# Optimization experiments

Measured on AMD Instinct MI355X. Metric: run time of the kernel, lower is better.

## Reference

```python
import jax, jax.numpy as jnp
import numpy as np

HIDDEN = 2048
NUM_HEADS = 16
HEAD_DIM = 128
CHUNK = 256
TOPK = 4
THETA = 10000.0
SCALE = HEAD_DIM ** -0.5


def _rope(x, pos):
    # x: [S, H, D], pos: [S] int. NeoX-style rotate-half (vLLM get_rope default).
    half = HEAD_DIM // 2
    inv = 1.0 / (THETA ** (jnp.arange(half, dtype=jnp.float32) / half))
    ang = pos.astype(jnp.float32)[:, None] * inv          # [S, half]
    cos = jnp.cos(ang)[:, None, :]                        # [S, 1, half]
    sin = jnp.sin(ang)[:, None, :]
    x1, x2 = x[..., :half], x[..., half:]
    return jnp.concatenate([x1 * cos - x2 * sin, x2 * cos + x1 * sin], axis=-1)


def _moba_attn(q, k, v):
    # q, k, v: [S, H, D]; causal MoBA block-sparse attention for one sequence.
    S, H, D = q.shape
    N = S // CHUNK
    # mean-pooled key gate per chunk: [N, H, D]
    key_gate = k.reshape(N, CHUNK, H, D).mean(axis=1)
    gate = jnp.einsum('shd,nhd->shn', q, key_gate)        # [S, H, N]
    cq = jnp.arange(S) // CHUNK                           # chunk index of each query
    n_idx = jnp.arange(N)
    neg = jnp.finfo(gate.dtype).min
    future = (n_idx[None, :] > cq[:, None])[:, None, :]   # [S, 1, N]
    selfc = (n_idx[None, :] == cq[:, None])[:, None, :]
    gate = jnp.where(future, neg, gate)
    gate = jnp.where(selfc, jnp.inf, gate)                # self chunk always selected
    k_sel = min(TOPK, N)
    _, idx = jax.lax.top_k(gate, k_sel)                   # [S, H, k]
    sel = jax.nn.one_hot(idx, N, dtype=jnp.float32).sum(axis=-2) > 0  # [S, H, N] bool
    # expand chunk selection to per-key mask and combine with causal mask
    chunk_of_t = jnp.arange(S) // CHUNK
    sel_full = sel[:, :, chunk_of_t]                      # [S, H, S]
    causal = (jnp.arange(S)[None, :] <= jnp.arange(S)[:, None])[:, None, :]
    allow = causal & sel_full
    scores = jnp.einsum('shd,thd->sht', q, k) * SCALE     # [S, H, S]
    scores = jnp.where(allow, scores, neg)
    p = jax.nn.softmax(scores, axis=-1)
    return jnp.einsum('sht,thd->shd', p, v)


def setup_inputs() -> dict:
    key = jax.random.key(0)
    k1, k2, k3 = jax.random.split(key, 3)
    B, S = 2, 2048
    hidden_states = jax.random.normal(k1, (B, S, HIDDEN), dtype=jnp.float32)
    positions = jnp.tile(jnp.arange(S, dtype=jnp.int32)[None, :], (B, 1))
    qkv_w = jax.random.normal(k2, (3 * NUM_HEADS * HEAD_DIM, HIDDEN), dtype=jnp.float32) * 0.02
    o_w = jax.random.normal(k3, (HIDDEN, NUM_HEADS * HEAD_DIM), dtype=jnp.float32) * 0.02
    return {'hidden_states': hidden_states, 'positions': positions, 'qkv_w': qkv_w, 'o_w': o_w}


def reference(hidden_states, positions, qkv_w, o_w):
    B, S, _ = hidden_states.shape
    qkv = jnp.einsum('bsi,oi->bso', hidden_states, qkv_w)  # [B, S, 3*H*D]
    q, k, v = jnp.split(qkv, 3, axis=-1)
    q = q.reshape(B, S, NUM_HEADS, HEAD_DIM)
    k = k.reshape(B, S, NUM_HEADS, HEAD_DIM)
    v = v.reshape(B, S, NUM_HEADS, HEAD_DIM)
    q = jax.vmap(_rope)(q, positions)
    k = jax.vmap(_rope)(k, positions)
    o = jax.vmap(_moba_attn)(q, k, v)                      # [B, S, H, D]
    o = o.reshape(B, S, NUM_HEADS * HEAD_DIM)
    return jnp.einsum('bsd,od->bso', o, o_w)
```

## Files before the change

### kernel.cpp

```cpp
#include <hip/hip_runtime.h>
#include <hip/hip_bf16.h>
#include <math.h>
#include <string.h>

#define SEQ     2048
#define NHEAD   16
#define HDIM    128
#define HIDDEN  2048
#define QKV_N   6144
#define CHUNKSZ 256
#define NCHUNK  8
#define SCALE_F 0.08838834764831845f
#define NEGBIG  -1e30f

typedef unsigned short u16;
typedef unsigned int   u32;
typedef _Float16       f16;
typedef __attribute__((ext_vector_type(8))) short    s16x8;
typedef __attribute__((ext_vector_type(8))) _Float16 f16x8;
typedef __attribute__((ext_vector_type(4))) float    f32x4;

__device__ __forceinline__ u16 f2bf(float x) {
  __hip_bfloat16 h = __float2bfloat16(x);
  u16 r; memcpy(&r, &h, 2); return r;
}
__device__ __forceinline__ float bf2f(u16 u) {
  u32 b = (u32)u << 16; float f; memcpy(&f, &b, 4); return f;
}

__global__ __launch_bounds__(256) void prep_fl(const float* __restrict__ src,
                                               f16* __restrict__ hi,
                                               f16* __restrict__ lo) {
  int idx = blockIdx.x * 256 + threadIdx.x;
  int l  = idx & 63;
  int ks = (idx >> 6) & 63;
  int mt = idx >> 12;
  const float* sp = src + (size_t)(mt * 16 + (l & 15)) * 2048 + ks * 32 + (l >> 4) * 8;
  float4 a = *(const float4*)sp;
  float4 b = *(const float4*)(sp + 4);
  float xs[8] = {a.x, a.y, a.z, a.w, b.x, b.y, b.z, b.w};
  f16x8 hv, lv;
#pragma unroll
  for (int j = 0; j < 8; ++j) {
    _Float16 h = (_Float16)xs[j];
    hv[j] = h;
    lv[j] = (_Float16)((xs[j] - (float)h) * 2048.0f);
  }
  size_t d = (size_t)idx * 8;
  *(f16x8*)&hi[d] = hv;
  *(f16x8*)&lo[d] = lv;
}

__global__ __launch_bounds__(256, 2) void gemm_fl(
    const f16* __restrict__ Ah, const f16* __restrict__ Al,
    const f16* __restrict__ Bh, const f16* __restrict__ Bl,
    float* __restrict__ C, int ldC, int coff) {
  __shared__ __align__(16) f16 sA[2][8][512];
  __shared__ __align__(16) f16 sB[2][8][512];
  const int tid = threadIdx.x;
  const int w = tid >> 6, lane = tid & 63;
  const int wr = w >> 1, wc = w & 1;
  const int lr = lane & 15, lg = lane >> 4;
  const int bm8 = blockIdx.y * 8;
  const int bn8 = blockIdx.x * 8;

  const f16* gmat = (w == 0) ? Ah : (w == 1) ? Al : (w == 2) ? Bh : Bl;
  const int  base8 = (w < 2) ? bm8 : bn8;
  f16* lmat = (w == 0) ? &sA[0][0][0] : (w == 1) ? &sA[1][0][0]
            : (w == 2) ? &sB[0][0][0] : &sB[1][0][0];
  const f16* gw = gmat + (size_t)lane * 8;
  f16* lw = lmat + lane * 8;

  f32x4 accH[4][4], accX[4][4];
#pragma unroll
  for (int i = 0; i < 4; ++i)
#pragma unroll
    for (int j = 0; j < 4; ++j) {
      accH[i][j] = (f32x4){0.f, 0.f, 0.f, 0.f};
      accX[i][j] = (f32x4){0.f, 0.f, 0.f, 0.f};
    }

  for (int ks = 0; ks < 64; ++ks) {
    f16x8 stg[8];
#pragma unroll
    for (int i = 0; i < 8; ++i)
      stg[i] = *(const f16x8*)(gw + (((size_t)(base8 + i) * 64 + ks) << 9));
    __syncthreads();
#pragma unroll
    for (int i = 0; i < 8; ++i)
      *(f16x8*)(lw + (i << 9)) = stg[i];
    __syncthreads();

    f16x8 ah[4], al[4], bh[4], bl[4];
#pragma unroll
    for (int i = 0; i < 4; ++i) {
      ah[i] = *(const f16x8*)&sA[0][wr * 4 + i][lane * 8];
      al[i] = *(const f16x8*)&sA[1][wr * 4 + i][lane * 8];
      bh[i] = *(const f16x8*)&sB[0][wc * 4 + i][lane * 8];
      bl[i] = *(const f16x8*)&sB[1][wc * 4 + i][lane * 8];
    }
#pragma unroll
    for (int i = 0; i < 4; ++i)
#pragma unroll
      for (int j = 0; j < 4; ++j) {
        accH[i][j] = __builtin_amdgcn_mfma_f32_16x16x32_f16(ah[i], bh[j], accH[i][j], 0, 0, 0);
        accX[i][j] = __builtin_amdgcn_mfma_f32_16x16x32_f16(al[i], bh[j], accX[i][j], 0, 0, 0);
        accX[i][j] = __builtin_amdgcn_mfma_f32_16x16x32_f16(ah[i], bl[j], accX[i][j], 0, 0, 0);
      }
  }

#pragma unroll
  for (int i = 0; i < 4; ++i) {
    const int row0 = blockIdx.y * 128 + wr * 64 + i * 16 + lg * 4;
    const int col0 = coff + blockIdx.x * 128 + wc * 64 + lr;
#pragma unroll
    for (int r = 0; r < 4; ++r) {
      float* cp = C + (size_t)(row0 + r) * ldC + col0;
#pragma unroll
      for (int j = 0; j < 4; ++j)
        cp[j * 16] = accH[i][j][r] + accX[i][j][r] * 4.8828125e-4f;
    }
  }
}

__global__ __launch_bounds__(256) void rope_inplace(float* __restrict__ qkv,
                                                    const int* __restrict__ pos) {
  int idx = blockIdx.x * 256 + threadIdx.x;
  int j = idx & 63;
  int h = (idx >> 6) & 15;
  int s = (idx >> 10) & (SEQ - 1);
  int b = idx >> 21;
  float p = (float)pos[b * SEQ + s];
  float inv = (float)exp(-(double)j * 1.4391156831212787e-1);
  float ang = p * inv;
  float sn = sinf(ang);
  float cs = cosf(ang);
  size_t row = (size_t)(b * SEQ + s) * QKV_N;
  float* qp = qkv + row + h * HDIM;
  float x1 = qp[j], x2 = qp[j + 64];
  qp[j] = x1 * cs - x2 * sn;
  qp[j + 64] = x2 * cs + x1 * sn;
  float* kp = qkv + row + HIDDEN + h * HDIM;
  x1 = kp[j]; x2 = kp[j + 64];
  kp[j] = x1 * cs - x2 * sn;
  kp[j + 64] = x2 * cs + x1 * sn;
}

__global__ __launch_bounds__(128) void key_gate_k(const float* __restrict__ qkv,
                                                  float* __restrict__ kg) {
  int bhn = blockIdx.x;
  int d = threadIdx.x;
  int n = bhn & 7;
  int bh = bhn >> 3;
  int b = bh >> 4, h = bh & 15;
  const float* kp = qkv + (size_t)(b * SEQ + n * CHUNKSZ) * QKV_N + HIDDEN + h * HDIM + d;
  float sum = 0.f;
  for (int i = 0; i < CHUNKSZ; ++i) sum += kp[(size_t)i * QKV_N];
  kg[(size_t)bh * NCHUNK * HDIM + n * HDIM + d] = sum * (1.f / CHUNKSZ);
}

__global__ __launch_bounds__(256) void gate_topk(const float* __restrict__ qkv,
                                                 const float* __restrict__ kg,
                                                 unsigned char* __restrict__ msk) {
  int gw = (blockIdx.x * 256 + threadIdx.x) >> 6;
  int lane = threadIdx.x & 63;
  int s = gw & (SEQ - 1);
  int bh = gw >> 11;
  int b = bh >> 4, h = bh & 15;
  int cq = s >> 8;
  const float* qp = qkv + (size_t)(b * SEQ + s) * QKV_N + h * HDIM;
  float q0 = qp[lane], q1 = qp[lane + 64];
  const float* kgp = kg + (size_t)bh * NCHUNK * HDIM;
  float g[7];
#pragma unroll
  for (int n = 0; n < 7; ++n) {
    float part = 0.f;
    if (n < cq) part = q0 * kgp[n * HDIM + lane] + q1 * kgp[n * HDIM + lane + 64];
#pragma unroll
    for (int off = 32; off > 0; off >>= 1) part += __shfl_xor(part, off);
    g[n] = part;
  }
  unsigned m = 1u << cq;
  int nsel = cq < 3 ? cq : 3;
#pragma unroll
  for (int it = 0; it < 3; ++it) {
    int best = -1; float bv = 0.f;
#pragma unroll
    for (int n = 0; n < 7; ++n) {
      bool cand = (n < cq) && !((m >> n) & 1u);
      if (cand && (best < 0 || g[n] > bv)) { bv = g[n]; best = n; }
    }
    if (it < nsel) m |= 1u << best;
  }
  if (lane == 0) msk[gw] = (unsigned char)m;
}

__global__ __launch_bounds__(256) void prep_k(const float* __restrict__ qkv,
                                              u16* __restrict__ khi,
                                              u16* __restrict__ klo) {
  int idx = blockIdx.x * 256 + threadIdx.x;
  int lane = idx & 63;
  int ds = (idx >> 6) & 3;
  int kt = (idx >> 8) & 127;
  int bh = idx >> 15;
  int b = bh >> 4, h = bh & 15;
  int s = kt * 16 + (lane & 15);
  int d = ds * 32 + (lane >> 4) * 8;
  const float* src = qkv + (size_t)(b * SEQ + s) * QKV_N + HIDDEN + h * HDIM + d;
  float4 a = *(const float4*)src;
  float4 c = *(const float4*)(src + 4);
  float xs[8] = {a.x, a.y, a.z, a.w, c.x, c.y, c.z, c.w};
  s16x8 hi, lo;
#pragma unroll
  for (int j = 0; j < 8; ++j) {
    u16 hb = f2bf(xs[j]);
    hi[j] = (short)hb;
    lo[j] = (short)f2bf(xs[j] - bf2f(hb));
  }
  size_t dst = (size_t)idx * 8;
  *(s16x8*)&khi[dst] = hi;
  *(s16x8*)&klo[dst] = lo;
}

__global__ __launch_bounds__(256) void prep_v(const float* __restrict__ qkv,
                                              u16* __restrict__ vhi,
                                              u16* __restrict__ vlo) {
  int idx = blockIdx.x * 256 + threadIdx.x;
  int lane = idx & 63;
  int ts = (idx >> 6) & 63;
  int dt = (idx >> 12) & 7;
  int bh = idx >> 15;
  int b = bh >> 4, h = bh & 15;
  int t = ts * 32 + (lane >> 4) * 8;
  int d = dt * 16 + (lane & 15);
  const float* src = qkv + (size_t)(b * SEQ + t) * QKV_N + 2 * HIDDEN + h * HDIM + d;
  s16x8 hi, lo;
#pragma unroll
  for (int j = 0; j < 8; ++j) {
    float x = src[(size_t)j * QKV_N];
    u16 hb = f2bf(x);
    hi[j] = (short)hb;
    lo[j] = (short)f2bf(x - bf2f(hb));
  }
  size_t dst = (size_t)idx * 8;
  *(s16x8*)&vhi[dst] = hi;
  *(s16x8*)&vlo[dst] = lo;
}

#define PSTRIDE 40
__global__ __launch_bounds__(256) void moba_attn_mfma(
    const float* __restrict__ qkv,
    const u16* __restrict__ khi, const u16* __restrict__ klo,
    const u16* __restrict__ vhi, const u16* __restrict__ vlo,
    const unsigned char* __restrict__ msk, float* __restrict__ o) {
  __shared__ u16 KHI[4096], KLO[4096];
  __shared__ u16 VHI[4096], VLO[4096];
  __shared__ u16 PHI[4][16 * PSTRIDE], PLO[4][16 * PSTRIDE];
  __shared__ unsigned char Ms[64];
  __shared__ unsigned bm_sh;

  const int qt = blockIdx.x, h = blockIdx.y, b = blockIdx.z;
  const int tid = threadIdx.x;
  const int w = tid >> 6, lane = tid & 63;
  const int lr = lane & 15, lg = lane >> 4;
  const int bh = b * NHEAD + h;
  const int q0g = qt * 64;
  const int q0w = q0g + w * 16;
  const int cq = qt >> 2;

  if (tid < 64) Ms[tid] = msk[(size_t)bh * SEQ + q0g + tid];
  __syncthreads();
  if (tid == 0) {
    unsigned m = 0;
    for (int i = 0; i < 64; ++i) m |= Ms[i];
    bm_sh = m;
  }

  s16x8 qh[4], ql[4];
  {
    const float* qp = qkv + (size_t)(b * SEQ + q0w + lr) * QKV_N + h * HDIM + lg * 8;
#pragma unroll
    for (int ds = 0; ds < 4; ++ds) {
      float4 a = *(const float4*)(qp + ds * 32);
      float4 c = *(const float4*)(qp + ds * 32 + 4);
      float xs[8] = {a.x, a.y, a.z, a.w, c.x, c.y, c.z, c.w};
      s16x8 hi, lo;
#pragma unroll
      for (int j = 0; j < 8; ++j) {
        u16 hb = f2bf(xs[j]);
        hi[j] = (short)hb;
        lo[j] = (short)f2bf(xs[j] - bf2f(hb));
      }
      qh[ds] = hi; ql[ds] = lo;
    }
  }
  __syncthreads();
  const unsigned bmask = bm_sh;

  int qrow[4]; unsigned char rowm[4];
#pragma unroll
  for (int r = 0; r < 4; ++r) {
    qrow[r] = q0w + lg * 4 + r;
    rowm[r] = Ms[w * 16 + lg * 4 + r];
  }

  float m_run[4], l_run[4];
  f32x4 Oacc[8];
#pragma unroll
  for (int r = 0; r < 4; ++r) { m_run[r] = NEGBIG; l_run[r] = 0.f; }
#pragma unroll
  for (int dt = 0; dt < 8; ++dt) Oacc[dt] = (f32x4){0.f, 0.f, 0.f, 0.f};

  for (int n = 0; n <= cq; ++n) {
    if (!((bmask >> n) & 1u)) continue;
    const int nk = (n == cq) ? ((qt & 3) * 64 + 64) : CHUNKSZ;
    for (int t0 = n * CHUNKSZ; t0 < n * CHUNKSZ + nk; t0 += 32) {
      __syncthreads();
      if (w < 2) {
        const u16* src = (w == 0 ? khi : klo) +
                         ((size_t)bh * 128 + (t0 >> 4)) * 2048 + lane * 8;
        u16* dst = (w == 0 ? KHI : KLO);
#pragma unroll
        for (int i = 0; i < 8; ++i)
          *(s16x8*)&dst[i * 512 + lane * 8] = *(const s16x8*)(src + i * 512);
      } else {
        const u16* src = (w == 2 ? vhi : vlo) +
                         ((size_t)bh * 8 * 64 + (t0 >> 5)) * 512 + lane * 8;
        u16* dst = (w == 2 ? VHI : VLO);
#pragma unroll
        for (int dt = 0; dt < 8; ++dt)
          *(s16x8*)&dst[dt * 512 + lane * 8] = *(const s16x8*)(src + (size_t)dt * 32768);
      }
      __syncthreads();

      f32x4 acc[2];
      acc[0] = (f32x4){0.f, 0.f, 0.f, 0.f};
      acc[1] = (f32x4){0.f, 0.f, 0.f, 0.f};
#pragma unroll
      for (int kt = 0; kt < 2; ++kt)
#pragma unroll
        for (int ds = 0; ds < 4; ++ds) {
          s16x8 bhf = *(const s16x8*)&KHI[(kt * 4 + ds) * 512 + lane * 8];
          s16x8 blf = *(const s16x8*)&KLO[(kt * 4 + ds) * 512 + lane * 8];
          acc[kt] = __builtin_amdgcn_mfma_f32_16x16x32_bf16(qh[ds], bhf, acc[kt], 0, 0, 0);
          acc[kt] = __builtin_amdgcn_mfma_f32_16x16x32_bf16(ql[ds], bhf, acc[kt], 0, 0, 0);
          acc[kt] = __builtin_amdgcn_mfma_f32_16x16x32_bf16(qh[ds], blf, acc[kt], 0, 0, 0);
        }

      const int tg0 = t0 + lr, tg1 = t0 + 16 + lr;
      float alpha[4], p0v[4], p1v[4];
#pragma unroll
      for (int r = 0; r < 4; ++r) {
        bool okm = (rowm[r] >> n) & 1;
        float a0 = (okm && tg0 <= qrow[r]) ? acc[0][r] * SCALE_F : NEGBIG;
        float a1 = (okm && tg1 <= qrow[r]) ? acc[1][r] * SCALE_F : NEGBIG;
        float mx = fmaxf(a0, a1);
        mx = fmaxf(mx, __shfl_xor(mx, 1));
        mx = fmaxf(mx, __shfl_xor(mx, 2));
        mx = fmaxf(mx, __shfl_xor(mx, 4));
        mx = fmaxf(mx, __shfl_xor(mx, 8));
        float mnew = fmaxf(m_run[r], mx);
        float al = __expf(m_run[r] - mnew);
        float p0 = __expf(a0 - mnew);
        float p1 = __expf(a1 - mnew);
        float ps = p0 + p1;
        ps += __shfl_xor(ps, 1);
        ps += __shfl_xor(ps, 2);
        ps += __shfl_xor(ps, 4);
        ps += __shfl_xor(ps, 8);
        l_run[r] = l_run[r] * al + ps;
        m_run[r] = mnew;
        alpha[r] = al; p0v[r] = p0; p1v[r] = p1;
      }
      f32x4 av = {alpha[0], alpha[1], alpha[2], alpha[3]};
#pragma unroll
      for (int dt = 0; dt < 8; ++dt) Oacc[dt] *= av;

#pragma unroll
      for (int r = 0; r < 4; ++r) {
        int row = lg * 4 + r;
        u16 h0 = f2bf(p0v[r]);
        u16 h1 = f2bf(p1v[r]);
        PHI[w][row * PSTRIDE + lr]      = h0;
        PHI[w][row * PSTRIDE + 16 + lr] = h1;
        PLO[w][row * PSTRIDE + lr]      = f2bf(p0v[r] - bf2f(h0));
        PLO[w][row * PSTRIDE + 16 + lr] = f2bf(p1v[r] - bf2f(h1));
      }
      s16x8 pah = *(const s16x8*)&PHI[w][lr * PSTRIDE + lg * 8];
      s16x8 pal = *(const s16x8*)&PLO[w][lr * PSTRIDE + lg * 8];
#pragma unroll
      for (int dt = 0; dt < 8; ++dt) {
        s16x8 vbh = *(const s16x8*)&VHI[dt * 512 + lane * 8];
        s16x8 vbl = *(const s16x8*)&VLO[dt * 512 + lane * 8];
        Oacc[dt] = __builtin_amdgcn_mfma_f32_16x16x32_bf16(pah, vbh, Oacc[dt], 0, 0, 0);
        Oacc[dt] = __builtin_amdgcn_mfma_f32_16x16x32_bf16(pal, vbh, Oacc[dt], 0, 0, 0);
        Oacc[dt] = __builtin_amdgcn_mfma_f32_16x16x32_bf16(pah, vbl, Oacc[dt], 0, 0, 0);
      }
    }
  }

  float inv[4];
#pragma unroll
  for (int r = 0; r < 4; ++r) inv[r] = 1.f / l_run[r];
#pragma unroll
  for (int dt = 0; dt < 8; ++dt)
#pragma unroll
    for (int r = 0; r < 4; ++r)
      o[(size_t)(b * SEQ + qrow[r]) * HIDDEN + h * HDIM + dt * 16 + lr] =
          Oacc[dt][r] * inv[r];
}

extern "C" void kernel_launch(void* const* d_in, const int* in_sizes, int n_in,
                              void* d_out, int out_size, void* d_ws, size_t ws_size,
                              hipStream_t stream) {
  const float* hs    = (const float*)d_in[0];
  const int*   pos   = (const int*)d_in[1];
  const float* w_qkv = (const float*)d_in[2];
  const float* w_o   = (const float*)d_in[3];
  float* out = (float*)d_out;

  char* ws = (char*)d_ws;
  float* qkv = (float*)ws;
  float* o   = (float*)(ws + 100663296);
  float* kg  = (float*)(ws + 134217728);
  unsigned char* msk = (unsigned char*)(ws + 134348800);
  char* rx   = ws + 134414336;
  f16* Ah = (f16*)rx;
  f16* Al = (f16*)(rx + 16777216);
  f16* Bh = (f16*)(rx + 33554432);
  f16* Bl = (f16*)(rx + 41943040);
  u16* khi = (u16*)rx;
  u16* klo = (u16*)(rx + 16777216);
  u16* vhi = (u16*)(rx + 33554432);
  u16* vlo = (u16*)(rx + 50331648);

  prep_fl<<<4096, 256, 0, stream>>>(hs, Ah, Al);
  for (int i = 0; i < 3; ++i) {
    prep_fl<<<2048, 256, 0, stream>>>(w_qkv + (size_t)i * 2048 * 2048, Bh, Bl);
    gemm_fl<<<dim3(16, 32), 256, 0, stream>>>(Ah, Al, Bh, Bl, qkv, QKV_N, i * 2048);
  }
  rope_inplace<<<16384, 256, 0, stream>>>(qkv, pos);
  key_gate_k<<<2 * NHEAD * NCHUNK, 128, 0, stream>>>(qkv, kg);
  gate_topk<<<16384, 256, 0, stream>>>(qkv, kg, msk);
  prep_k<<<4096, 256, 0, stream>>>(qkv, khi, klo);
  prep_v<<<4096, 256, 0, stream>>>(qkv, vhi, vlo);
  moba_attn_mfma<<<dim3(SEQ / 64, NHEAD, 2), 256, 0, stream>>>(qkv, khi, klo,
                                                               vhi, vlo, msk, o);
  prep_fl<<<4096, 256, 0, stream>>>(o, Ah, Al);
  prep_fl<<<2048, 256, 0, stream>>>(w_o, Bh, Bl);
  gemm_fl<<<dim3(16, 32), 256, 0, stream>>>(Ah, Al, Bh, Bl, out, HIDDEN, 0);
}
```

Measured before the change: 972.6 us.

## Prefetch next K/V tile into registers, remap attention grid for XCD locality

```diff
diff --git a/kernel.cpp b/kernel.cpp
--- a/kernel.cpp
+++ b/kernel.cpp
@@ -259,7 +259,13 @@
   __shared__ unsigned char Ms[64];
   __shared__ unsigned bm_sh;
 
-  const int qt = blockIdx.x, h = blockIdx.y, b = blockIdx.z;
+  const int L = blockIdx.x;
+  const int xcd = L & 7;
+  const int t = L >> 3;
+  const int qt = 31 - (t & 31);
+  const int g = (t >> 5) * 8 + xcd;
+  const int b = g >> 4, h = g & 15;
+
   const int tid = threadIdx.x;
   const int w = tid >> 6, lane = tid & 63;
   const int lr = lane & 15, lg = lane >> 4;
@@ -267,6 +273,7 @@
   const int q0g = qt * 64;
   const int q0w = q0g + w * 16;
   const int cq = qt >> 2;
+  const int dk = (qt & 3) * 64 + 64;
 
   if (tid < 64) Ms[tid] = msk[(size_t)bh * SEQ + q0g + tid];
   __syncthreads();
@@ -311,92 +318,124 @@
 #pragma unroll
   for (int dt = 0; dt < 8; ++dt) Oacc[dt] = (f32x4){0.f, 0.f, 0.f, 0.f};
 
-  for (int n = 0; n <= cq; ++n) {
-    if (!((bmask >> n) & 1u)) continue;
-    const int nk = (n == cq) ? ((qt & 3) * 64 + 64) : CHUNKSZ;
-    for (int t0 = n * CHUNKSZ; t0 < n * CHUNKSZ + nk; t0 += 32) {
-      __syncthreads();
+  u16* ldst = (w == 0) ? KHI : (w == 1) ? KLO : (w == 2) ? VHI : VLO;
+
+  int n = 0;
+  while (!((bmask >> n) & 1u)) ++n;
+  int kt = 0;
+  s16x8 stg[8];
+  {
+    const int t0 = n * CHUNKSZ + kt;
+    if (w < 2) {
+      const u16* src = (w == 0 ? khi : klo) + ((size_t)bh * 128 + (t0 >> 4)) * 2048 + lane * 8;
+#pragma unroll
+      for (int i = 0; i < 8; ++i) stg[i] = *(const s16x8*)(src + i * 512);
+    } else {
+      const u16* src = (w == 2 ? vhi : vlo) + ((size_t)bh * 8 * 64 + (t0 >> 5)) * 512 + lane * 8;
+#pragma unroll
+      for (int i = 0; i < 8; ++i) stg[i] = *(const s16x8*)(src + (size_t)i * 32768);
+    }
+  }
+
+  for (;;) {
+    __syncthreads();
+#pragma unroll
+    for (int i = 0; i < 8; ++i)
+      *(s16x8*)&ldst[i * 512 + lane * 8] = stg[i];
+    __syncthreads();
+
+    int n2 = n, kt2 = kt + 32;
+    const int nk = (n == cq) ? dk : CHUNKSZ;
+    if (kt2 >= nk) {
+      n2 = -1; kt2 = 0;
+      for (int m = n + 1; m <= cq; ++m)
+        if ((bmask >> m) & 1u) { n2 = m; break; }
+    }
+    if (n2 >= 0) {
+      const int t0n = n2 * CHUNKSZ + kt2;
       if (w < 2) {
-        const u16* src = (w == 0 ? khi : klo) +
-                         ((size_t)bh * 128 + (t0 >> 4)) * 2048 + lane * 8;
-        u16* dst = (w == 0 ? KHI : KLO);
-#pragma unroll
-        for (int i = 0; i < 8; ++i)
-          *(s16x8*)&dst[i * 512 + lane * 8] = *(const s16x8*)(src + i * 512);
+        const u16* src = (w == 0 ? khi : klo) + ((size_t)bh * 128 + (t0n >> 4)) * 2048 + lane * 8;
+#pragma unroll
+        for (int i = 0; i < 8; ++i) stg[i] = *(const s16x8*)(src + i * 512);
       } else {
-        const u16* src = (w == 2 ? vhi : vlo) +
-                         ((size_t)bh * 8 * 64 + (t0 >> 5)) * 512 + lane * 8;
-        u16* dst = (w == 2 ? VHI : VLO);
-#pragma unroll
-        for (int dt = 0; dt < 8; ++dt)
-          *(s16x8*)&dst[dt * 512 + lane * 8] = *(const s16x8*)(src + (size_t)dt * 32768);
+        const u16* src = (w == 2 ? vhi : vlo) + ((size_t)bh * 8 * 64 + (t0n >> 5)) * 512 + lane * 8;
+#pragma unroll
+        for (int i = 0; i < 8; ++i) stg[i] = *(const s16x8*)(src + (size_t)i * 32768);
       }
-      __syncthreads();
-
-      f32x4 acc[2];
-      acc[0] = (f32x4){0.f, 0.f, 0.f, 0.f};
-      acc[1] = (f32x4){0.f, 0.f, 0.f, 0.f};
-#pragma unroll
-      for (int kt = 0; kt < 2; ++kt)
-#pragma unroll
-        for (int ds = 0; ds < 4; ++ds) {
-          s16x8 bhf = *(const s16x8*)&KHI[(kt * 4 + ds) * 512 + lane * 8];
-          s16x8 blf = *(const s16x8*)&KLO[(kt * 4 + ds) * 512 + lane * 8];
-          acc[kt] = __builtin_amdgcn_mfma_f32_16x16x32_bf16(qh[ds], bhf, acc[kt], 0, 0, 0);
-          acc[kt] = __builtin_amdgcn_mfma_f32_16x16x32_bf16(ql[ds], bhf, acc[kt], 0, 0, 0);
-          acc[kt] = __builtin_amdgcn_mfma_f32_16x16x32_bf16(qh[ds], blf, acc[kt], 0, 0, 0);
-        }
-
-      const int tg0 = t0 + lr, tg1 = t0 + 16 + lr;
-      float alpha[4], p0v[4], p1v[4];
-#pragma unroll
-      for (int r = 0; r < 4; ++r) {
-        bool okm = (rowm[r] >> n) & 1;
-        float a0 = (okm && tg0 <= qrow[r]) ? acc[0][r] * SCALE_F : NEGBIG;
-        float a1 = (okm && tg1 <= qrow[r]) ? acc[1][r] * SCALE_F : NEGBIG;
-        float mx = fmaxf(a0, a1);
-        mx = fmaxf(mx, __shfl_xor(mx, 1));
-        mx = fmaxf(mx, __shfl_xor(mx, 2));
-        mx = fmaxf(mx, __shfl_xor(mx, 4));
-        mx = fmaxf(mx, __shfl_xor(mx, 8));
-        float mnew = fmaxf(m_run[r], mx);
-        float al = __expf(m_run[r] - mnew);
-        float p0 = __expf(a0 - mnew);
-        float p1 = __expf(a1 - mnew);
-        float ps = p0 + p1;
-        ps += __shfl_xor(ps, 1);
-        ps += __shfl_xor(ps, 2);
-        ps += __shfl_xor(ps, 4);
-        ps += __shfl_xor(ps, 8);
-        l_run[r] = l_run[r] * al + ps;
-        m_run[r] = mnew;
-        alpha[r] = al; p0v[r] = p0; p1v[r] = p1;
+    }
+
+    const int t0 = n * CHUNKSZ + kt;
+
+    f32x4 acc[2];
+    acc[0] = (f32x4){0.f, 0.f, 0.f, 0.f};
+    acc[1] = (f32x4){0.f, 0.f, 0.f, 0.f};
+    __builtin_amdgcn_s_setprio(1);
+#pragma unroll
+    for (int ktt = 0; ktt < 2; ++ktt)
+#pragma unroll
+      for (int ds = 0; ds < 4; ++ds) {
+        s16x8 bhf = *(const s16x8*)&KHI[(ktt * 4 + ds) * 512 + lane * 8];
+        s16x8 blf = *(const s16x8*)&KLO[(ktt * 4 + ds) * 512 + lane * 8];
+        acc[ktt] = __builtin_amdgcn_mfma_f32_16x16x32_bf16(qh[ds], bhf, acc[ktt], 0, 0, 0);
+        acc[ktt] = __builtin_amdgcn_mfma_f32_16x16x32_bf16(ql[ds], bhf, acc[ktt], 0, 0, 0);
+        acc[ktt] = __builtin_amdgcn_mfma_f32_16x16x32_bf16(qh[ds], blf, acc[ktt], 0, 0, 0);
       }
-      f32x4 av = {alpha[0], alpha[1], alpha[2], alpha[3]};
-#pragma unroll
-      for (int dt = 0; dt < 8; ++dt) Oacc[dt] *= av;
-
-#pragma unroll
-      for (int r = 0; r < 4; ++r) {
-        int row = lg * 4 + r;
-        u16 h0 = f2bf(p0v[r]);
-        u16 h1 = f2bf(p1v[r]);
-        PHI[w][row * PSTRIDE + lr]      = h0;
-        PHI[w][row * PSTRIDE + 16 + lr] = h1;
-        PLO[w][row * PSTRIDE + lr]      = f2bf(p0v[r] - bf2f(h0));
-        PLO[w][row * PSTRIDE + 16 + lr] = f2bf(p1v[r] - bf2f(h1));
-      }
-      s16x8 pah = *(const s16x8*)&PHI[w][lr * PSTRIDE + lg * 8];
-      s16x8 pal = *(const s16x8*)&PLO[w][lr * PSTRIDE + lg * 8];
-#pragma unroll
-      for (int dt = 0; dt < 8; ++dt) {
-        s16x8 vbh = *(const s16x8*)&VHI[dt * 512 + lane * 8];
-        s16x8 vbl = *(const s16x8*)&VLO[dt * 512 + lane * 8];
-        Oacc[dt] = __builtin_amdgcn_mfma_f32_16x16x32_bf16(pah, vbh, Oacc[dt], 0, 0, 0);
-        Oacc[dt] = __builtin_amdgcn_mfma_f32_16x16x32_bf16(pal, vbh, Oacc[dt], 0, 0, 0);
-        Oacc[dt] = __builtin_amdgcn_mfma_f32_16x16x32_bf16(pah, vbl, Oacc[dt], 0, 0, 0);
-      }
-    }
+    __builtin_amdgcn_s_setprio(0);
+
+    const int tg0 = t0 + lr, tg1 = t0 + 16 + lr;
+    float alpha[4], p0v[4], p1v[4];
+#pragma unroll
+    for (int r = 0; r < 4; ++r) {
+      bool okm = (rowm[r] >> n) & 1;
+      float a0 = (okm && tg0 <= qrow[r]) ? acc[0][r] * SCALE_F : NEGBIG;
+      float a1 = (okm && tg1 <= qrow[r]) ? acc[1][r] * SCALE_F : NEGBIG;
+      float mx = fmaxf(a0, a1);
+      mx = fmaxf(mx, __shfl_xor(mx, 1));
+      mx = fmaxf(mx, __shfl_xor(mx, 2));
+      mx = fmaxf(mx, __shfl_xor(mx, 4));
+      mx = fmaxf(mx, __shfl_xor(mx, 8));
+      float mnew = fmaxf(m_run[r], mx);
+      float al = __expf(m_run[r] - mnew);
+      float p0 = __expf(a0 - mnew);
+      float p1 = __expf(a1 - mnew);
+      float ps = p0 + p1;
+      ps += __shfl_xor(ps, 1);
+      ps += __shfl_xor(ps, 2);
+      ps += __shfl_xor(ps, 4);
+      ps += __shfl_xor(ps, 8);
+      l_run[r] = l_run[r] * al + ps;
+      m_run[r] = mnew;
+      alpha[r] = al; p0v[r] = p0; p1v[r] = p1;
+    }
+    f32x4 av = {alpha[0], alpha[1], alpha[2], alpha[3]};
+#pragma unroll
+    for (int dt = 0; dt < 8; ++dt) Oacc[dt] *= av;
+
+#pragma unroll
+    for (int r = 0; r < 4; ++r) {
+      int row = lg * 4 + r;
+      u16 h0 = f2bf(p0v[r]);
+      u16 h1 = f2bf(p1v[r]);
+      PHI[w][row * PSTRIDE + lr]      = h0;
+      PHI[w][row * PSTRIDE + 16 + lr] = h1;
+      PLO[w][row * PSTRIDE + lr]      = f2bf(p0v[r] - bf2f(h0));
+      PLO[w][row * PSTRIDE + 16 + lr] = f2bf(p1v[r] - bf2f(h1));
+    }
+    s16x8 pah = *(const s16x8*)&PHI[w][lr * PSTRIDE + lg * 8];
+    s16x8 pal = *(const s16x8*)&PLO[w][lr * PSTRIDE + lg * 8];
+    __builtin_amdgcn_s_setprio(1);
+#pragma unroll
+    for (int dt = 0; dt < 8; ++dt) {
+      s16x8 vbh = *(const s16x8*)&VHI[dt * 512 + lane * 8];
+      s16x8 vbl = *(const s16x8*)&VLO[dt * 512 + lane * 8];
+      Oacc[dt] = __builtin_amdgcn_mfma_f32_16x16x32_bf16(pah, vbh, Oacc[dt], 0, 0, 0);
+      Oacc[dt] = __builtin_amdgcn_mfma_f32_16x16x32_bf16(pal, vbh, Oacc[dt], 0, 0, 0);
+      Oacc[dt] = __builtin_amdgcn_mfma_f32_16x16x32_bf16(pah, vbl, Oacc[dt], 0, 0, 0);
+    }
+    __builtin_amdgcn_s_setprio(0);
+
+    if (n2 < 0) break;
+    n = n2; kt = kt2;
   }
 
   float inv[4];
@@ -444,8 +483,8 @@
   gate_topk<<<16384, 256, 0, stream>>>(qkv, kg, msk);
   prep_k<<<4096, 256, 0, stream>>>(qkv, khi, klo);
   prep_v<<<4096, 256, 0, stream>>>(qkv, vhi, vlo);
-  moba_attn_mfma<<<dim3(SEQ / 64, NHEAD, 2), 256, 0, stream>>>(qkv, khi, klo,
-                                                               vhi, vlo, msk, o);
+  moba_attn_mfma<<<dim3(1024), 256, 0, stream>>>(qkv, khi, klo,
+                                                 vhi, vlo, msk, o);
   prep_fl<<<4096, 256, 0, stream>>>(o, Ah, Al);
   prep_fl<<<2048, 256, 0, stream>>>(w_o, Bh, Bl);
   gemm_fl<<<dim3(16, 32), 256, 0, stream>>>(Ah, Al, Bh, Bl, out, HIDDEN, 0);
```

Measured after the change: 882.3 us. 1.1x faster.
